# Kernel optimization log

Measured on AMD Instinct MI355X. Metric: run time of the kernel, lower is better.

Reference implementation:

```python
import jax, jax.numpy as jnp
import numpy as np

HEADS = 16  # init_kwargs['heads']


def setup_inputs() -> dict:
    key = jax.random.key(0)
    k1, k2, k3, k4, k5, k6 = jax.random.split(key, 6)
    N, L, E = 2, 2048, 1024
    return {
        "values": jax.random.normal(k1, (N, L, E), dtype=jnp.float32),
        "key": jax.random.normal(k2, (N, L, E), dtype=jnp.float32),
        "query": jax.random.normal(k3, (N, L, E), dtype=jnp.float32),
        "mask": jax.random.randint(k4, (N, 1, L, L), 0, 2, dtype=jnp.int32),
        # fc_out: Linear(heads*head_dim=E, E) with bias
        "W_out": jax.random.normal(k5, (E, E), dtype=jnp.float32) / np.sqrt(E),
        "b_out": jax.random.normal(k6, (E,), dtype=jnp.float32) * 0.01,
    }


def reference(values, key, query, mask, W_out, b_out):
    N, Lq, E = query.shape
    Lk = key.shape[1]
    H = HEADS
    D = E // H  # head_dim = 64
    q = query.reshape(N, Lq, H, D)
    k = key.reshape(N, Lk, H, D)
    v = values.reshape(N, Lk, H, D)
    # energy: (N, H, Q, K)
    energy = jnp.einsum("nqhd,nkhd->nhqk", q, k)
    # masked_fill BEFORE scaling, as in the original
    energy = jnp.where(mask == 0, jnp.float32(-1e20), energy)
    attn = jax.nn.softmax(energy / np.float32(np.sqrt(D)), axis=3)
    out = jnp.einsum("nhqk,nkhd->nqhd", attn, v).reshape(N, Lq, H * D)
    return out @ W_out.T + b_out
```

## Files before the change

### kernel.cpp

```cpp
#include <hip/hip_runtime.h>

#define L_SEQ  2048
#define EMB    1024
#define NHEAD  16
#define HDIM   64
#define NBATCH 2
#define NT     (L_SEQ / 64)

typedef unsigned short u16;
typedef unsigned int   u32;
typedef unsigned long long u64;
typedef short bf16x8 __attribute__((ext_vector_type(8)));
typedef float f32x4  __attribute__((ext_vector_type(4)));
typedef int   i32x4  __attribute__((ext_vector_type(4)));

static __device__ __forceinline__ u16 f2bf(float x) {
    union { float f; unsigned u; } a; a.f = x;
    unsigned r = a.u + 0x7FFFu + ((a.u >> 16) & 1u);
    return (u16)(r >> 16);
}
static __device__ __forceinline__ void cvt8(const float4& a, const float4& b, u16* o, float s) {
    o[0]=f2bf(a.x*s); o[1]=f2bf(a.y*s); o[2]=f2bf(a.z*s); o[3]=f2bf(a.w*s);
    o[4]=f2bf(b.x*s); o[5]=f2bf(b.y*s); o[6]=f2bf(b.z*s); o[7]=f2bf(b.w*s);
}

static __device__ __forceinline__ u32 cvt_pk_bf16(float lo, float hi) {
    u32 r;
    asm("v_cvt_pk_bf16_f32 %0, %1, %2" : "=v"(r) : "v"(lo), "v"(hi));
    return r;
}
static __device__ __forceinline__ void permswap32(u32 &x, u32 &y) {
    asm("v_permlane32_swap_b32 %0, %1" : "+v"(x), "+v"(y));
}
static __device__ __forceinline__ void permswap16(u32 &x, u32 &y) {
    asm("v_permlane16_swap_b32 %0, %1" : "+v"(x), "+v"(y));
}

__global__ __launch_bounds__(256)
void prep_fused(const float* __restrict__ Qg, const float* __restrict__ Kg,
                const float* __restrict__ Vg, const int* __restrict__ Mg,
                const float* __restrict__ Wg,
                u16* __restrict__ Qb, u16* __restrict__ Kb, u16* __restrict__ Vt,
                u64* __restrict__ maskp, u16* __restrict__ Wb)
{
    const int bid = blockIdx.x;
    const int tid = threadIdx.x;
    __shared__ u16 Vl2[64][72];

    if (bid < 1024) {
        const int wave = tid >> 6;
        const int lane = tid & 63;
        const int row  = bid * 4 + wave;
        const int* mp = Mg + (size_t)row * L_SEQ + lane;
        u64* op = maskp + (size_t)row * NT;
        for (int tt = 0; tt < NT; ++tt) {
            u64 b = __ballot(mp[tt * 64] != 0);
            if (lane == 0) op[tt] = b;
        }
    } else if (bid < 2048) {
        const int b  = bid - 1024;
        const int tt = b & 31, hh = (b >> 5) & 15, nn = b >> 9;
        const int row = tid >> 2;
        const int dc  = (tid & 3) * 16;

        const size_t gin = ((size_t)(nn * L_SEQ) + tt * 64 + row) * EMB + hh * HDIM + dc;

        {
            const float qs = 0.125f * 1.44269504f;
            u16 o[16];
            cvt8(*(const float4*)(Qg + gin),     *(const float4*)(Qg + gin + 4),  o,     qs);
            cvt8(*(const float4*)(Qg + gin + 8), *(const float4*)(Qg + gin + 12), o + 8, qs);
            *(uint4*)(Qb + gin)     = *(const uint4*)o;
            *(uint4*)(Qb + gin + 8) = *(const uint4*)&o[8];
        }
        {
            u16 o[16];
            cvt8(*(const float4*)(Kg + gin),     *(const float4*)(Kg + gin + 4),  o,     1.f);
            cvt8(*(const float4*)(Kg + gin + 8), *(const float4*)(Kg + gin + 12), o + 8, 1.f);
            size_t ko = ((size_t)(nn * NHEAD + hh) * L_SEQ + tt * 64 + row) * HDIM + dc;
            *(uint4*)(Kb + ko)     = *(const uint4*)o;
            *(uint4*)(Kb + ko + 8) = *(const uint4*)&o[8];
        }
        {
            u16 o[16];
            cvt8(*(const float4*)(Vg + gin),     *(const float4*)(Vg + gin + 4),  o,     1.f);
            cvt8(*(const float4*)(Vg + gin + 8), *(const float4*)(Vg + gin + 12), o + 8, 1.f);
            #pragma unroll
            for (int j = 0; j < 16; ++j) Vl2[dc + j][row] = o[j];
        }
        __syncthreads();
        {
            const int d  = tid >> 2;
            const int kc = (tid & 3) * 16;
            size_t vo = ((size_t)(nn * NHEAD + hh) * HDIM + d) * L_SEQ + tt * 64 + kc;
            *(uint4*)(Vt + vo)     = *(const uint4*)&Vl2[d][kc];
            *(uint4*)(Vt + vo + 8) = *(const uint4*)&Vl2[d][kc + 8];
        }
    } else {
        int i = ((bid - 2048) * 256 + tid) * 8;
        float4 a = *(const float4*)(Wg + i);
        float4 b4 = *(const float4*)(Wg + i + 4);
        u16 o[8];
        cvt8(a, b4, o, 1.f);
        *(uint4*)(Wb + i) = *(const uint4*)o;
    }
}

static __device__ __forceinline__ void pv_step(
    const u32 (&Dwp)[2][8], const u16 (&Vb)[64][72],
    f32x4 (&acc)[2][4], int l16, int quad)
{
    #pragma unroll
    for (int kc = 0; kc < 2; ++kc) {
        bf16x8 pf[2];
        #pragma unroll
        for (int qs = 0; qs < 2; ++qs) {
            u32 b0 = Dwp[qs][4 * kc + 0], b2 = Dwp[qs][4 * kc + 2];
            permswap32(b0, b2); permswap16(b0, b2);
            u32 b1 = Dwp[qs][4 * kc + 1], b3 = Dwp[qs][4 * kc + 3];
            permswap32(b1, b3); permswap16(b1, b3);
            union { i32x4 i; bf16x8 v; } pu;
            pu.i[0] = (int)b0; pu.i[1] = (int)b1; pu.i[2] = (int)b2; pu.i[3] = (int)b3;
            pf[qs] = pu.v;
        }
        #pragma unroll
        for (int dc = 0; dc < 4; ++dc) {
            bf16x8 vf = *(const bf16x8*)&Vb[dc * 16 + l16][kc * 32 + quad * 8];
            acc[0][dc] = __builtin_amdgcn_mfma_f32_16x16x32_bf16(vf, pf[0], acc[0][dc], 0, 0, 0);
            acc[1][dc] = __builtin_amdgcn_mfma_f32_16x16x32_bf16(vf, pf[1], acc[1][dc], 0, 0, 0);
        }
    }
}

static __device__ __forceinline__ void attn_tile(
    int t, int kbuf, int vprev, int kw, int vw,
    u32 (&Dwc)[2][8], u32 (&Dwp)[2][8],
    u16 (&Kl)[2][64][72], u16 (&Vl)[4][64][72],
    const bf16x8 (&qf)[2][2], f32x4 (&acc)[2][4], float (&ls)[2][4],
    uint4& kr0, uint4& kr1, uint4& vr0, uint4& vr1,
    u64& mr0, u64& mr1,
    const u16* kbase, const u16* vbase, const u64* mbase, int mqs,
    int srow, int scol, int l16, int quad)
{
    if (t < NT - 1) {
        *(uint4*)&Kl[kw][srow][scol]     = kr0;
        *(uint4*)&Kl[kw][srow][scol + 8] = kr1;
        *(uint4*)&Vl[vw][srow][scol]     = vr0;
        *(uint4*)&Vl[vw][srow][scol + 8] = vr1;
    }
    u64 mcur0 = mr0, mcur1 = mr1;
    if (t < NT - 1) { mr0 = mbase[t + 1]; mr1 = mbase[mqs + t + 1]; }
    if (t < NT - 2) {
        const u16* kp = kbase + (size_t)((t + 2) * 64 + srow) * HDIM + scol;
        const u16* vp = vbase + (size_t)srow * L_SEQ + (t + 2) * 64 + scol;
        kr0 = *(const uint4*)kp;  kr1 = *(const uint4*)(kp + 8);
        vr0 = *(const uint4*)vp;  vr1 = *(const uint4*)(vp + 8);
    }

    const int sh = quad * 4;
    u32 mlo0 = (u32)mcur0 >> sh, mhi0 = (u32)(mcur0 >> 32) >> sh;
    u32 mlo1 = (u32)mcur1 >> sh, mhi1 = (u32)(mcur1 >> 32) >> sh;
    #pragma unroll
    for (int cc = 0; cc < 4; ++cc) {
        bf16x8 k0 = *(const bf16x8*)&Kl[kbuf][cc * 16 + l16][quad * 8];
        bf16x8 k1 = *(const bf16x8*)&Kl[kbuf][cc * 16 + l16][32 + quad * 8];
        f32x4 z0; z0[0]=0.f; z0[1]=0.f; z0[2]=0.f; z0[3]=0.f;
        f32x4 z1 = z0;
        z0 = __builtin_amdgcn_mfma_f32_16x16x32_bf16(k0, qf[0][0], z0, 0, 0, 0);
        z0 = __builtin_amdgcn_mfma_f32_16x16x32_bf16(k1, qf[0][1], z0, 0, 0, 0);
        z1 = __builtin_amdgcn_mfma_f32_16x16x32_bf16(k0, qf[1][0], z1, 0, 0, 0);
        z1 = __builtin_amdgcn_mfma_f32_16x16x32_bf16(k1, qf[1][1], z1, 0, 0, 0);

        #pragma unroll
        for (int qs = 0; qs < 2; ++qs) {
            const f32x4& z = (qs == 0) ? z0 : z1;
            u32 w = (cc < 2) ? ((qs == 0) ? mlo0 : mlo1)
                             : ((qs == 0) ? mhi0 : mhi1);
            float pv[4];
            #pragma unroll
            for (int r = 0; r < 4; ++r) {
                const int pos = (cc & 1) * 16 + r;
                int sm = (int)(w << (31 - pos)) >> 31;
                float p = __builtin_amdgcn_exp2f(z[r]);
                p = __int_as_float(__float_as_int(p) & sm);
                ls[qs][r] += p;
                pv[r] = p;
            }
            Dwc[qs][2 * cc]     = cvt_pk_bf16(pv[0], pv[1]);
            Dwc[qs][2 * cc + 1] = cvt_pk_bf16(pv[2], pv[3]);
        }
    }

    pv_step(Dwp, Vl[vprev], acc, l16, quad);

    __syncthreads();
}

__global__ __launch_bounds__(256, 2)
void attn_kernel(const u16* __restrict__ Qb, const u16* __restrict__ Kb,
                 const u16* __restrict__ Vt, const u64* __restrict__ maskp,
                 u16* __restrict__ Og)
{
    const int qblk = blockIdx.x;
    const int h    = blockIdx.y;
    const int n    = blockIdx.z;
    const int tid  = threadIdx.x;
    const int wave = tid >> 6;
    const int lane = tid & 63;
    const int l16  = lane & 15;
    const int quad = lane >> 4;

    __shared__ u16 Kl[2][64][72];
    __shared__ u16 Vl[4][64][72];

    const int q0 = qblk * 128 + wave * 32;

    bf16x8 qf[2][2];
    #pragma unroll
    for (int qs = 0; qs < 2; ++qs) {
        const u16* qp = Qb + ((size_t)(n * L_SEQ) + q0 + qs * 16 + l16) * EMB + h * HDIM;
        qf[qs][0] = *(const bf16x8*)(qp + quad * 8);
        qf[qs][1] = *(const bf16x8*)(qp + 32 + quad * 8);
    }

    f32x4 acc[2][4];
    #pragma unroll
    for (int qs = 0; qs < 2; ++qs)
        #pragma unroll
        for (int c = 0; c < 4; ++c)
            #pragma unroll
            for (int r = 0; r < 4; ++r) acc[qs][c][r] = 0.f;
    float ls[2][4];
    #pragma unroll
    for (int qs = 0; qs < 2; ++qs)
        #pragma unroll
        for (int r = 0; r < 4; ++r) ls[qs][r] = 0.f;

    u32 DwA[2][8], DwB[2][8];
    #pragma unroll
    for (int qs = 0; qs < 2; ++qs)
        #pragma unroll
        for (int i = 0; i < 8; ++i) { DwA[qs][i] = 0u; DwB[qs][i] = 0u; }

    const u16* kbase = Kb + (size_t)(n * NHEAD + h) * L_SEQ * HDIM;
    const u16* vbase = Vt + (size_t)(n * NHEAD + h) * HDIM * L_SEQ;
    const u64* mbase = maskp + ((size_t)(n * L_SEQ) + q0 + l16) * NT;
    const int  mqs   = 16 * NT;

    const int srow = tid >> 2;
    const int scol = (tid & 3) * 16;

    uint4 kr0, kr1, vr0, vr1;
    u64 mr0, mr1;

    {
        const u16* kp = kbase + (size_t)srow * HDIM + scol;
        const u16* vp = vbase + (size_t)srow * L_SEQ + scol;
        kr0 = *(const uint4*)kp;  kr1 = *(const uint4*)(kp + 8);
        vr0 = *(const uint4*)vp;  vr1 = *(const uint4*)(vp + 8);
    }
    *(uint4*)&Kl[0][srow][scol]     = kr0;
    *(uint4*)&Kl[0][srow][scol + 8] = kr1;
    *(uint4*)&Vl[0][srow][scol]     = vr0;
    *(uint4*)&Vl[0][srow][scol + 8] = vr1;
    {
        u32* vz = (u32*)&Vl[3][0][0];
        #pragma unroll
        for (int i = 0; i < 9; ++i) vz[tid + i * 256] = 0u;
    }
    {
        const u16* kp = kbase + (size_t)(64 + srow) * HDIM + scol;
        const u16* vp = vbase + (size_t)srow * L_SEQ + 64 + scol;
        kr0 = *(const uint4*)kp;  kr1 = *(const uint4*)(kp + 8);
        vr0 = *(const uint4*)vp;  vr1 = *(const uint4*)(vp + 8);
    }
    mr0 = mbase[0];
    mr1 = mbase[mqs];
    __syncthreads();

    for (int j = 0; j < 8; ++j) {
        const int t = j * 4;
        attn_tile(t + 0, 0, 3, 1, 1, DwA, DwB, Kl, Vl, qf, acc, ls,
                  kr0, kr1, vr0, vr1, mr0, mr1, kbase, vbase, mbase, mqs,
                  srow, scol, l16, quad);
        attn_tile(t + 1, 1, 0, 0, 2, DwB, DwA, Kl, Vl, qf, acc, ls,
                  kr0, kr1, vr0, vr1, mr0, mr1, kbase, vbase, mbase, mqs,
                  srow, scol, l16, quad);
        attn_tile(t + 2, 0, 1, 1, 3, DwA, DwB, Kl, Vl, qf, acc, ls,
                  kr0, kr1, vr0, vr1, mr0, mr1, kbase, vbase, mbase, mqs,
                  srow, scol, l16, quad);
        attn_tile(t + 3, 1, 2, 0, 0, DwB, DwA, Kl, Vl, qf, acc, ls,
                  kr0, kr1, vr0, vr1, mr0, mr1, kbase, vbase, mbase, mqs,
                  srow, scol, l16, quad);
    }

    pv_step(DwB, Vl[3], acc, l16, quad);

    #pragma unroll
    for (int qs = 0; qs < 2; ++qs) {
        float s = (ls[qs][0] + ls[qs][1]) + (ls[qs][2] + ls[qs][3]);
        s += __shfl_xor(s, 16);
        s += __shfl_xor(s, 32);
        float inv = 1.f / s;

        u16* op = Og + ((size_t)(n * L_SEQ) + q0 + qs * 16 + l16) * EMB + h * HDIM + quad * 4;
        #pragma unroll
        for (int dc = 0; dc < 4; ++dc) {
            u32 u0 = cvt_pk_bf16(acc[qs][dc][0] * inv, acc[qs][dc][1] * inv);
            u32 u1 = cvt_pk_bf16(acc[qs][dc][2] * inv, acc[qs][dc][3] * inv);
            uint2 st; st.x = u0; st.y = u1;
            *(uint2*)(op + dc * 16) = st;
        }
    }
}

__global__ __launch_bounds__(256, 4)
void out_gemm(const u16* __restrict__ A, const u16* __restrict__ B,
              const float* __restrict__ bias, float* __restrict__ out)
{
    const int bn  = blockIdx.x;
    const int bm  = blockIdx.y;
    const int tid = threadIdx.x;
    const int wave = tid >> 6;
    const int lane = tid & 63;
    const int l16  = lane & 15;
    const int quad = lane >> 4;
    const int wr = wave >> 1, wc = wave & 1;

    __shared__ u16 Al[64][72];
    __shared__ u16 Bl[64][72];

    f32x4 acc[2][2];
    #pragma unroll
    for (int i = 0; i < 2; ++i)
        #pragma unroll
        for (int j = 0; j < 2; ++j)
            #pragma unroll
            for (int r = 0; r < 4; ++r) acc[i][j][r] = 0.f;

    const int srow = tid >> 2;
    const int kc   = (tid & 3) * 16;

    const u16* ap = A + (size_t)(bm * 64 + srow) * EMB + kc;
    const u16* bp = B + (size_t)(bn * 64 + srow) * EMB + kc;

    uint4 ar0 = *(const uint4*)ap,        ar1 = *(const uint4*)(ap + 8);
    uint4 br0 = *(const uint4*)bp,        br1 = *(const uint4*)(bp + 8);

    for (int k0 = 0; k0 < EMB; k0 += 64) {
        __syncthreads();
        *(uint4*)&Al[srow][kc]     = ar0;
        *(uint4*)&Al[srow][kc + 8] = ar1;
        *(uint4*)&Bl[srow][kc]     = br0;
        *(uint4*)&Bl[srow][kc + 8] = br1;
        if (k0 + 64 < EMB) {
            ar0 = *(const uint4*)(ap + k0 + 64);  ar1 = *(const uint4*)(ap + k0 + 72);
            br0 = *(const uint4*)(bp + k0 + 64);  br1 = *(const uint4*)(bp + k0 + 72);
        }
        __syncthreads();

        #pragma unroll
        for (int kk = 0; kk < 2; ++kk) {
            bf16x8 af[2], bfr[2];
            #pragma unroll
            for (int i = 0; i < 2; ++i)
                af[i] = *(const bf16x8*)&Al[wr * 32 + i * 16 + l16][kk * 32 + quad * 8];
            #pragma unroll
            for (int j = 0; j < 2; ++j)
                bfr[j] = *(const bf16x8*)&Bl[wc * 32 + j * 16 + l16][kk * 32 + quad * 8];
            #pragma unroll
            for (int i = 0; i < 2; ++i)
                #pragma unroll
                for (int j = 0; j < 2; ++j)
                    acc[i][j] = __builtin_amdgcn_mfma_f32_16x16x32_bf16(af[i], bfr[j], acc[i][j], 0, 0, 0);
        }
    }

    #pragma unroll
    for (int j = 0; j < 2; ++j) {
        int col = bn * 64 + wc * 32 + j * 16 + l16;
        float bv = bias[col];
        #pragma unroll
        for (int i = 0; i < 2; ++i) {
            int row0 = bm * 64 + wr * 32 + i * 16 + quad * 4;
            #pragma unroll
            for (int r = 0; r < 4; ++r)
                out[(size_t)(row0 + r) * EMB + col] = acc[i][j][r] + bv;
        }
    }
}

extern "C" void kernel_launch(void* const* d_in, const int* in_sizes, int n_in,
                              void* d_out, int out_size, void* d_ws, size_t ws_size,
                              hipStream_t stream)
{
    const float* Vg = (const float*)d_in[0];
    const float* Kg = (const float*)d_in[1];
    const float* Qg = (const float*)d_in[2];
    const int*   Mg = (const int*)d_in[3];
    const float* Wg = (const float*)d_in[4];
    const float* Bg = (const float*)d_in[5];
    float* Og = (float*)d_out;

    const size_t QKV = (size_t)NBATCH * L_SEQ * EMB;
    char* ws = (char*)d_ws;
    u16* attn_ws = (u16*)ws;
    u16* Wb      = (u16*)(ws + QKV * 2);
    u16* Qb      = (u16*)(ws + QKV * 2 + 2 * 1024 * 1024);
    u16* Kb      = Qb + QKV;
    u16* Vt      = Kb + QKV;
    u64* maskp   = (u64*)(Vt + QKV);

    prep_fused<<<dim3(2560), 256, 0, stream>>>(Qg, Kg, Vg, Mg, Wg,
                                               Qb, Kb, Vt, maskp, Wb);

    dim3 g1(L_SEQ / 128, NHEAD, NBATCH);
    attn_kernel<<<g1, 256, 0, stream>>>(Qb, Kb, Vt, maskp, attn_ws);

    dim3 g2(EMB / 64, (NBATCH * L_SEQ) / 64);
    out_gemm<<<g2, 256, 0, stream>>>(attn_ws, Wb, Bg, Og);
}
```

Before: 204.4 us.

## Swizzle block order, use lightweight LDS barriers, raise priority during PV MFMAs

Replaces the 3D grids of the attention and output GEMM kernels with 1D grids remapped so groups of 8 consecutive blocks share K/V heads or A rows, aiming for better L2 reuse across the chiplet-interleaved dispatch. __syncthreads is replaced by an explicit lgkmcnt wait plus s_barrier and a scheduling barrier, which avoids waiting on outstanding global loads (vmcnt) at each barrier. The PV MFMA section runs at raised wave priority. The explicit barrier relies on the prefetched global loads not needing completion before the barrier; the scheduling barrier may also restrict compiler reordering.

After: 207.0 us. About the same (+1.3%).

```diff
diff --git a/kernel.cpp b/kernel.cpp
--- a/kernel.cpp
+++ b/kernel.cpp
@@ -34,6 +34,12 @@
 }
 static __device__ __forceinline__ void permswap16(u32 &x, u32 &y) {
     asm("v_permlane16_swap_b32 %0, %1" : "+v"(x), "+v"(y));
+}
+
+static __device__ __forceinline__ void lds_barrier() {
+    asm volatile("s_waitcnt lgkmcnt(0)" ::: "memory");
+    __builtin_amdgcn_s_barrier();
+    __builtin_amdgcn_sched_barrier(0);
 }
 
 __global__ __launch_bounds__(256)
@@ -110,6 +116,7 @@
     const u32 (&Dwp)[2][8], const u16 (&Vb)[64][72],
     f32x4 (&acc)[2][4], int l16, int quad)
 {
+    __builtin_amdgcn_s_setprio(1);
     #pragma unroll
     for (int kc = 0; kc < 2; ++kc) {
         bf16x8 pf[2];
@@ -130,6 +137,7 @@
             acc[1][dc] = __builtin_amdgcn_mfma_f32_16x16x32_bf16(vf, pf[1], acc[1][dc], 0, 0, 0);
         }
     }
+    __builtin_amdgcn_s_setprio(0);
 }
 
 static __device__ __forceinline__ void attn_tile(
@@ -193,7 +201,7 @@
 
     pv_step(Dwp, Vl[vprev], acc, l16, quad);
 
-    __syncthreads();
+    lds_barrier();
 }
 
 __global__ __launch_bounds__(256, 2)
@@ -201,9 +209,14 @@
                  const u16* __restrict__ Vt, const u64* __restrict__ maskp,
                  u16* __restrict__ Og)
 {
-    const int qblk = blockIdx.x;
-    const int h    = blockIdx.y;
-    const int n    = blockIdx.z;
+    const int i    = blockIdx.x;
+    const int x    = i & 7;
+    const int s    = i >> 3;
+    const int g    = ((s >> 4) << 3) + x;
+    const int qblk = s & 15;
+    const int h    = g & 15;
+    const int n    = g >> 4;
+
     const int tid  = threadIdx.x;
     const int wave = tid >> 6;
     const int lane = tid & 63;
@@ -240,7 +253,7 @@
     #pragma unroll
     for (int qs = 0; qs < 2; ++qs)
         #pragma unroll
-        for (int i = 0; i < 8; ++i) { DwA[qs][i] = 0u; DwB[qs][i] = 0u; }
+        for (int ii = 0; ii < 8; ++ii) { DwA[qs][ii] = 0u; DwB[qs][ii] = 0u; }
 
     const u16* kbase = Kb + (size_t)(n * NHEAD + h) * L_SEQ * HDIM;
     const u16* vbase = Vt + (size_t)(n * NHEAD + h) * HDIM * L_SEQ;
@@ -266,7 +279,7 @@
     {
         u32* vz = (u32*)&Vl[3][0][0];
         #pragma unroll
-        for (int i = 0; i < 9; ++i) vz[tid + i * 256] = 0u;
+        for (int ii = 0; ii < 9; ++ii) vz[tid + ii * 256] = 0u;
     }
     {
         const u16* kp = kbase + (size_t)(64 + srow) * HDIM + scol;
@@ -298,10 +311,10 @@
 
     #pragma unroll
     for (int qs = 0; qs < 2; ++qs) {
-        float s = (ls[qs][0] + ls[qs][1]) + (ls[qs][2] + ls[qs][3]);
-        s += __shfl_xor(s, 16);
-        s += __shfl_xor(s, 32);
-        float inv = 1.f / s;
+        float sm = (ls[qs][0] + ls[qs][1]) + (ls[qs][2] + ls[qs][3]);
+        sm += __shfl_xor(sm, 16);
+        sm += __shfl_xor(sm, 32);
+        float inv = 1.f / sm;
 
         u16* op = Og + ((size_t)(n * L_SEQ) + q0 + qs * 16 + l16) * EMB + h * HDIM + quad * 4;
         #pragma unroll
@@ -318,8 +331,12 @@
 void out_gemm(const u16* __restrict__ A, const u16* __restrict__ B,
               const float* __restrict__ bias, float* __restrict__ out)
 {
-    const int bn  = blockIdx.x;
-    const int bm  = blockIdx.y;
+    const int i  = blockIdx.x;
+    const int x  = i & 7;
+    const int s  = i >> 3;
+    const int bm = ((s >> 4) << 3) + x;
+    const int bn = s & 15;
+
     const int tid = threadIdx.x;
     const int wave = tid >> 6;
     const int lane = tid & 63;
@@ -332,11 +349,11 @@
 
     f32x4 acc[2][2];
     #pragma unroll
-    for (int i = 0; i < 2; ++i)
+    for (int ii = 0; ii < 2; ++ii)
         #pragma unroll
         for (int j = 0; j < 2; ++j)
             #pragma unroll
-            for (int r = 0; r < 4; ++r) acc[i][j][r] = 0.f;
+            for (int r = 0; r < 4; ++r) acc[ii][j][r] = 0.f;
 
     const int srow = tid >> 2;
     const int kc   = (tid & 3) * 16;
@@ -348,7 +365,7 @@
     uint4 br0 = *(const uint4*)bp,        br1 = *(const uint4*)(bp + 8);
 
     for (int k0 = 0; k0 < EMB; k0 += 64) {
-        __syncthreads();
+        lds_barrier();
         *(uint4*)&Al[srow][kc]     = ar0;
         *(uint4*)&Al[srow][kc + 8] = ar1;
         *(uint4*)&Bl[srow][kc]     = br0;
@@ -357,22 +374,22 @@
             ar0 = *(const uint4*)(ap + k0 + 64);  ar1 = *(const uint4*)(ap + k0 + 72);
             br0 = *(const uint4*)(bp + k0 + 64);  br1 = *(const uint4*)(bp + k0 + 72);
         }
-        __syncthreads();
+        lds_barrier();
 
         #pragma unroll
         for (int kk = 0; kk < 2; ++kk) {
             bf16x8 af[2], bfr[2];
             #pragma unroll
-            for (int i = 0; i < 2; ++i)
-                af[i] = *(const bf16x8*)&Al[wr * 32 + i * 16 + l16][kk * 32 + quad * 8];
+            for (int ii = 0; ii < 2; ++ii)
+                af[ii] = *(const bf16x8*)&Al[wr * 32 + ii * 16 + l16][kk * 32 + quad * 8];
             #pragma unroll
             for (int j = 0; j < 2; ++j)
                 bfr[j] = *(const bf16x8*)&Bl[wc * 32 + j * 16 + l16][kk * 32 + quad * 8];
             #pragma unroll
-            for (int i = 0; i < 2; ++i)
+            for (int ii = 0; ii < 2; ++ii)
                 #pragma unroll
                 for (int j = 0; j < 2; ++j)
-                    acc[i][j] = __builtin_amdgcn_mfma_f32_16x16x32_bf16(af[i], bfr[j], acc[i][j], 0, 0, 0);
+                    acc[ii][j] = __builtin_amdgcn_mfma_f32_16x16x32_bf16(af[ii], bfr[j], acc[ii][j], 0, 0, 0);
         }
     }
 
@@ -381,11 +398,11 @@
         int col = bn * 64 + wc * 32 + j * 16 + l16;
         float bv = bias[col];
         #pragma unroll
-        for (int i = 0; i < 2; ++i) {
-            int row0 = bm * 64 + wr * 32 + i * 16 + quad * 4;
+        for (int ii = 0; ii < 2; ++ii) {
+            int row0 = bm * 64 + wr * 32 + ii * 16 + quad * 4;
             #pragma unroll
             for (int r = 0; r < 4; ++r)
-                out[(size_t)(row0 + r) * EMB + col] = acc[i][j][r] + bv;
+                out[(size_t)(row0 + r) * EMB + col] = acc[ii][j][r] + bv;
         }
     }
 }
@@ -414,9 +431,7 @@
     prep_fused<<<dim3(2560), 256, 0, stream>>>(Qg, Kg, Vg, Mg, Wg,
                                                Qb, Kb, Vt, maskp, Wb);
 
-    dim3 g1(L_SEQ / 128, NHEAD, NBATCH);
-    attn_kernel<<<g1, 256, 0, stream>>>(Qb, Kb, Vt, maskp, attn_ws);
-
-    dim3 g2(EMB / 64, (NBATCH * L_SEQ) / 64);
-    out_gemm<<<g2, 256, 0, stream>>>(attn_ws, Wb, Bg, Og);
-}
+    attn_kernel<<<dim3(512), 256, 0, stream>>>(Qb, Kb, Vt, maskp, attn_ws);
+
+    out_gemm<<<dim3(1024), 256, 0, stream>>>(attn_ws, Wb, Bg, Og);
+}
```
